# Kernel optimization log

Measured on AMD Instinct MI355X. Metric: run time of the kernel, lower is better.

The kernel has to match this reference:

```python
import jax, jax.numpy as jnp
import numpy as np
from jax.scipy.special import logsumexp

NEG = -1e9  # surrogate for -inf (keeps masking arithmetic and grads NaN-free)
ABSTRACT_PEN = 0.5


def setup_inputs() -> dict:
    key = jax.random.key(0)
    ks = jax.random.split(key, 5)
    B, T, b = 32, 256, 16
    action_logps = jax.nn.log_softmax(jax.random.normal(ks[0], (B, T, b)), axis=-1)
    stop_logps = jax.nn.log_softmax(jax.random.normal(ks[1], (B, T + 1, b, 2)), axis=-1)
    start_logps = jax.nn.log_softmax(jax.random.normal(ks[2], (B, T + 1, b)), axis=-1)
    causal_pens = jax.random.uniform(ks[3], (B, T + 1, T + 1, b))
    lengths = jax.random.randint(ks[4], (B,), 1, T + 1)
    masks = (jnp.arange(T)[None, :] < lengths[:, None]).astype(jnp.float32)
    return {"action_logps": action_logps, "stop_logps": stop_logps,
            "start_logps": start_logps, "causal_pens": causal_pens,
            "masks": masks, "lengths": lengths}


def _cc_loss(action_logps, stop_logps, start_logps, causal_pens, masks, lengths):
    B, T, b = action_logps.shape
    start_logps = start_logps - ABSTRACT_PEN
    stop_logps = stop_logps[..., ::-1]  # STOP_IX == 0 -> flip so index 1 = stop

    a_ts = jnp.swapaxes(action_logps, 0, 1)            # [T,B,b]
    stop_ts = jnp.swapaxes(stop_logps[:, 1:], 0, 1)    # [T,B,b,2]  stop_logps[:, t+1]
    start_ts = jnp.swapaxes(start_logps[:, :T], 0, 1)  # [T,B,b]
    m_ts = jnp.swapaxes(masks, 0, 1)                   # [T,B]

    # ---- cc_fw: f[t] has shape [B,b,t,2]; pad segment-start axis to T ----
    f0 = jnp.full((B, b, T, 2), NEG).at[:, 0, 0, 1].set(0.0)

    def fw_step(f_prev, xs):
        a_t, stop_t, start_t, t = xs
        # continue current option: positions < t-1
        cont = f_prev[..., 0:1] + a_t[:, :, None, None] + stop_t[:, :, None, :]
        # start a new option at position t-1
        seg = logsumexp(f_prev[..., 1], axis=(1, 2))  # [B]
        new_seg = seg[:, None, None] + start_t[:, :, None] + a_t[:, :, None] + stop_t  # [B,b,2]
        idx = jnp.arange(T)[None, None, :, None]
        f_t = jnp.where(idx == t - 1, new_seg[:, :, None, :], cont)
        return f_t, f_t

    _, F = jax.lax.scan(fw_step, f0, (a_ts, stop_ts, start_ts, jnp.arange(1, T + 1)))
    F_full = jnp.concatenate([f0[None], F], axis=0)  # [T+1,B,b,T,2]
    total_logp = logsumexp(F_full[lengths, jnp.arange(B)][..., 1], axis=(1, 2))  # [B]

    # ---- cc_bw ----
    fT = jnp.full((B, b, 2), NEG).at[:, :, 1].set(0.0)

    def bw_step(f_next, xs):
        a_t, stop_t, start_t, m_t = xs
        f0c = a_t + logsumexp(stop_t + f_next, axis=2)  # [B,b]
        f1c = logsumexp(start_t[:, :, None] + a_t[:, :, None] + stop_t + f_next, axis=(1, 2))  # [B]
        f_t = jnp.stack([f0c, jnp.broadcast_to(f1c[:, None], f0c.shape)], axis=-1)
        done = jnp.stack([jnp.full_like(f0c, NEG), jnp.zeros_like(f0c)], axis=-1)
        f_t = jnp.where(m_t[:, None, None] > 0, f_t, done)
        return f_t, f_t

    _, BW = jax.lax.scan(bw_step, fT, (a_ts, stop_ts, start_ts, m_ts), reverse=True)
    BW_full = jnp.concatenate([BW, fT[None]], axis=0)  # [T+1,B,b,2]

    # ---- causal-consistency penalty expectation ----
    # marginal[t-1, B, b, start] = fw f[t][...,1] + bw f[t][...,1]
    marg = F[..., 1] + BW_full[1:][..., 1][:, :, :, None]          # [T,B,b,T]
    probs = jnp.exp(marg - total_logp[None, :, None, None])        # padded starts -> 0
    # pen[t-1, B, b, start] = causal_pens[B, start, t, b]
    pen = jnp.transpose(causal_pens[:, :T, 1:, :], (2, 0, 3, 1))   # [T,B,b,T]
    total_cc = jnp.sum(jnp.sum(probs * pen, axis=(2, 3)) * m_ts)
    return jnp.stack([jnp.sum(total_logp), total_cc])


def reference(action_logps, stop_logps, start_logps, causal_pens, masks, lengths):
    return _cc_loss(action_logps, stop_logps, start_logps, causal_pens, masks, lengths)
```

## Files before the change

### kernel.cpp

```cpp
#include <hip/hip_runtime.h>

constexpr int B  = 32;
constexpr int T  = 256;
constexpr int NB = 16;
#define INVLN2 1.4426950408889634f
#define LN2    0.6931471805599453f
#define AP2    (0.5f * 1.4426950408889634f)

__device__ __forceinline__ float fexp2(float x) { return exp2f(x); }
__device__ __forceinline__ float flog2(float x) { return __log2f(x); }

template<int C>
__device__ __forceinline__ float dppmv(float x) {
    return __int_as_float(__builtin_amdgcn_update_dpp(
        0, __float_as_int(x), C, 0xF, 0xF, true));
}

__device__ __forceinline__ float sum16(float x) {
    x += dppmv<0xB1>(x);
    x += dppmv<0x4E>(x);
    x += dppmv<0x141>(x);
    x += dppmv<0x140>(x);
    return x;
}

__global__ __launch_bounds__(256) void scan_kernel(
    const float* __restrict__ act_g,
    const float* __restrict__ stp_g,
    const float* __restrict__ str_g,
    const int*   __restrict__ len_g,
    float* __restrict__ Wbuf,
    float* __restrict__ TLbuf,
    float* __restrict__ Ubuf,
    float* __restrict__ Vbuf,
    float* __restrict__ SSbuf,
    float* __restrict__ SBbuf)
{
    __shared__ float sm[16384];
    float* A0 = sm;
    float* A1 = sm + 4096;
    float* TB = sm + 8192;
    float* Cx = sm + 12288;
    float* Gs = TB;

    const int beta = blockIdx.x;
    const int tid  = threadIdx.x;

    const float4* a4 = (const float4*)(act_g + (size_t)beta * (T * NB));
    const float4* s4 = (const float4*)(stp_g + (size_t)beta * ((T + 1) * NB * 2) + 32);
    const float4* t4 = (const float4*)(str_g + (size_t)beta * ((T + 1) * NB));

    for (int i4 = tid; i4 < 1024; i4 += 256) {
        const int idx = i4 >> 2, q = i4 & 3;
        float4 a  = a4[i4];
        float4 sA = s4[idx * 8 + q * 2];
        float4 sB = s4[idx * 8 + q * 2 + 1];
        float4 st = t4[i4];
        float4 v0, v1, vt;
        v0.x = fexp2((a.x + sA.x) * INVLN2); v1.x = fexp2((a.x + sA.y) * INVLN2);
        v0.y = fexp2((a.y + sA.z) * INVLN2); v1.y = fexp2((a.y + sA.w) * INVLN2);
        v0.z = fexp2((a.z + sB.x) * INVLN2); v1.z = fexp2((a.z + sB.y) * INVLN2);
        v0.w = fexp2((a.w + sB.z) * INVLN2); v1.w = fexp2((a.w + sB.w) * INVLN2);
        vt.x = fexp2(st.x * INVLN2 - AP2); vt.y = fexp2(st.y * INVLN2 - AP2);
        vt.z = fexp2(st.z * INVLN2 - AP2); vt.w = fexp2(st.w * INVLN2 - AP2);
        ((float4*)A0)[i4] = v0;
        ((float4*)A1)[i4] = v1;
        ((float4*)TB)[i4] = vt;
    }
    __syncthreads();

    const int wid  = tid >> 6;
    const int lane = tid & 63;
    const int b    = lane & 15;
    const int L    = len_g[beta];

    if (wid == 0) {
        const float* A0b = A0 + b; const float* A1b = A1 + b; const float* TBb = TB + b;
        float2* ss = (float2*)(SSbuf + beta * 512);
        float E = TBb[0], Z = 0.f;
        float a0c = A0b[0],  a1c = A1b[0],  tbc = TBb[16];
        float a0n = A0b[16], a1n = A1b[16], tbn = TBb[32];
        for (int idx = 0; idx < 256; ++idx) {
            const int p = (idx + 2) & 255;
            float a0p = A0b[p * 16], a1p = A1b[p * 16], tbp = TBb[((idx + 3) & 255) * 16];
            float S = sum16(E * a0c);
            if (lane == 0) ss[idx] = make_float2(S, Z);
            if (idx < 255) {
                float En = E * a1c + S * tbc;
                unsigned e = (__float_as_uint(S) >> 23) & 0xFFu;
                E = En * __uint_as_float((254u - e) << 23);
                Z += (float)((int)e - 127);
            }
            a0c = a0n; a1c = a1n; tbc = tbn;
            a0n = a0p; a1n = a1p; tbn = tbp;
        }
    } else if (wid == 1) {
        const float* A0b = A0 + b; const float* A1b = A1 + b; const float* TBb = TB + b;
        float2* sb = (float2*)(SBbuf + beta * 512);
        float F0 = 0.f, F1 = 1.f, Z = 0.f;
        float a0c = A0b[255 * 16], a1c = A1b[255 * 16], tbc = TBb[255 * 16];
        float a0n = A0b[254 * 16], a1n = A1b[254 * 16], tbn = TBb[254 * 16];
        for (int i = 255; i >= 0; --i) {
            const int p = (i - 2) & 255;
            float a0p = A0b[p * 16], a1p = A1b[p * 16], tbp = TBb[p * 16];
            float F0n = a1c * F0 + a0c * F1;
            float F1n = sum16(tbc * F0n);
            if (lane == 0) sb[i] = make_float2(F1n, Z);
            const bool mk = (i < L);
            unsigned e = (__float_as_uint(F1n) >> 23) & 0xFFu;
            float    r = __uint_as_float((254u - e) << 23);
            F0 = mk ? F0n * r : 0.f;
            F1 = mk ? F1n * r : 1.f;
            Z  = mk ? Z + (float)((int)e - 127) : 0.f;
            a0c = a0n; a1c = a1n; tbc = tbn;
            a0n = a0p; a1n = a1p; tbn = tbp;
        }
    } else if (wid == 2) {
        const int seg = lane >> 4;
        const float* ap = act_g + (size_t)beta * 4096 + b;
        const float* sp = stp_g + (size_t)beta * 8224 + 32 + b * 2 + 1;
        float s = 0.f;
#pragma unroll 8
        for (int k = 0; k < 64; ++k) {
            const int idx = seg * 64 + k;
            s += (ap[idx * 16] + sp[idx * 32]) * INVLN2;
        }
        float inc = s;
        float u1 = __shfl_up(inc, 16); if (lane >= 16) inc += u1;
        float u2 = __shfl_up(inc, 32); if (lane >= 32) inc += u2;
        float run = inc - s;
#pragma unroll 8
        for (int k = 0; k < 64; ++k) {
            const int idx = seg * 64 + k;
            run += (ap[idx * 16] + sp[idx * 32]) * INVLN2;
            Cx[idx * 16 + b] = run;
        }
    }
    __syncthreads();

    {
        float2 sz = ((const float2*)(SSbuf + beta * 512))[tid];
        float G = flog2(sz.x) + sz.y;
        Gs[tid + 1] = G;
        if (tid == L - 1) TLbuf[beta] = G;
        if (tid >= 1) {
            float2 fz = ((const float2*)(SBbuf + beta * 512))[tid];
            Wbuf[beta * (T + 1) + tid] = (tid < L) ? flog2(fz.x) + fz.y : 0.f;
        } else {
            Wbuf[beta * (T + 1) + T] = 0.f;
        }
    }
    __syncthreads();

    float4* Ub4 = (float4*)(Ubuf + (size_t)beta * (T * NB));
    float4* Vb4 = (float4*)(Vbuf + (size_t)beta * ((T + 1) * NB));
    for (int i4 = tid; i4 < 1024; i4 += 256) {
        const int row = i4 >> 2, q = i4 & 3;
        float4 c  = ((const float4*)Cx)[i4];
        float4 sA = s4[row * 8 + q * 2];
        float4 sB = s4[row * 8 + q * 2 + 1];
        float4 V;
        V.x = c.x + (sA.x - sA.y) * INVLN2;
        V.y = c.y + (sA.z - sA.w) * INVLN2;
        V.z = c.z + (sB.x - sB.y) * INVLN2;
        V.w = c.w + (sB.z - sB.w) * INVLN2;
        Vb4[(row + 1) * 4 + q] = V;
        float4 st = t4[i4];
        float4 U;
        if (row == 0) {
            U.x = st.x * INVLN2 - AP2; U.y = st.y * INVLN2 - AP2;
            U.z = st.z * INVLN2 - AP2; U.w = st.w * INVLN2 - AP2;
        } else {
            float g = Gs[row];
            float4 cm = ((const float4*)Cx)[i4 - 4];
            U.x = g + st.x * INVLN2 - AP2 - cm.x;
            U.y = g + st.y * INVLN2 - AP2 - cm.y;
            U.z = g + st.z * INVLN2 - AP2 - cm.z;
            U.w = g + st.w * INVLN2 - AP2 - cm.w;
        }
        Ub4[i4] = U;
    }
}

__global__ __launch_bounds__(256) void cc_kernel(
    const float* __restrict__ pens,
    const int*   __restrict__ len_g,
    const float* __restrict__ Wbuf,
    const float* __restrict__ TLbuf,
    const float* __restrict__ Ubuf,
    const float* __restrict__ Vbuf,
    float* __restrict__ part)
{
    const int beta = blockIdx.x;
    const int t    = blockIdx.y + 1;
    const int tid  = threadIdx.x;
    const int pidx = blockIdx.y * B + beta;
    const int L    = len_g[beta];
    if (t > L) { if (tid == 0) part[pidx] = 0.f; return; }

    const float c0 = Wbuf[beta * (T + 1) + t] - TLbuf[beta];
    const float4* U4 = (const float4*)(Ubuf + (size_t)beta * (T * NB));
    const float4* P4 = (const float4*)(pens + (size_t)beta * ((size_t)(T+1)*(T+1)*NB)
                                            + (size_t)t * NB);
    const int q = tid & 3;
    float4 vq = ((const float4*)(Vbuf + (size_t)beta * ((T + 1) * NB) + t * NB))[q];
    vq.x += c0; vq.y += c0; vq.z += c0; vq.w += c0;

    float local = 0.f;
    const int n4 = t * 4;
    for (int i4 = tid; i4 < n4; i4 += 256) {
        const int tau = i4 >> 2;
        float4 u = U4[i4];
        float4 p = P4[(size_t)tau * ((T + 1) * 4) + (i4 & 3)];
        local += fexp2(u.x + vq.x) * p.x + fexp2(u.y + vq.y) * p.y
               + fexp2(u.z + vq.z) * p.z + fexp2(u.w + vq.w) * p.w;
    }
#pragma unroll
    for (int off = 1; off < 64; off <<= 1) local += __shfl_xor(local, off);
    __shared__ float red[4];
    if ((tid & 63) == 0) red[tid >> 6] = local;
    __syncthreads();
    if (tid == 0) part[pidx] = red[0] + red[1] + red[2] + red[3];
}

__global__ __launch_bounds__(256) void final_kernel(
    const float* __restrict__ part, const float* __restrict__ TLbuf,
    float* __restrict__ out)
{
    const int tid = threadIdx.x;
    const float4* p4 = (const float4*)part;
    float s = 0.f;
#pragma unroll
    for (int k = 0; k < 8; ++k) {
        float4 v = p4[tid + 256 * k];
        s += v.x + v.y + v.z + v.w;
    }
#pragma unroll
    for (int off = 1; off < 64; off <<= 1) s += __shfl_xor(s, off);
    __shared__ float red[4];
    if ((tid & 63) == 0) red[tid >> 6] = s;
    __syncthreads();
    if (tid == 0) out[1] = red[0] + red[1] + red[2] + red[3];

    float tl = (tid < 32) ? TLbuf[tid] : 0.f;
    if (tid < 64) {
#pragma unroll
        for (int off = 1; off < 32; off <<= 1) tl += __shfl_xor(tl, off);
        if (tid == 0) out[0] = tl * LN2;
    }
}

extern "C" void kernel_launch(void* const* d_in, const int* in_sizes, int n_in,
                              void* d_out, int out_size, void* d_ws, size_t ws_size,
                              hipStream_t stream) {
    (void)in_sizes; (void)n_in; (void)out_size; (void)ws_size;
    const float* act  = (const float*)d_in[0];
    const float* stp  = (const float*)d_in[1];
    const float* strt = (const float*)d_in[2];
    const float* pens = (const float*)d_in[3];
    const int*   lens = (const int*)d_in[5];
    float* out = (float*)d_out;

    float* ws    = (float*)d_ws;
    float* Wbuf  = ws;
    float* TLbuf = Wbuf + B * (T + 1);
    float* Ubuf  = TLbuf + B;
    float* Vbuf  = Ubuf + (size_t)B * T * NB;
    float* part  = Vbuf + (size_t)B * (T+1) * NB;
    float* SSbuf = part + T * B;
    float* SBbuf = SSbuf + B * 512;

    scan_kernel<<<B, 256, 0, stream>>>(act, stp, strt, lens, Wbuf, TLbuf, Ubuf, Vbuf, SSbuf, SBbuf);
    cc_kernel<<<dim3(B, T), 256, 0, stream>>>(pens, lens, Wbuf, TLbuf, Ubuf, Vbuf, part);
    final_kernel<<<1, 256, 0, stream>>>(part, TLbuf, out);
}
```

Before: 230.2 us.

## Merge cc blocks into 8-step chunks and drop final reduction kernel via atomics

The penalty kernel now assigns eight consecutive time steps to each block, cutting the grid from B×T to B×32 blocks and amortizing per-block setup. The separate final reduction kernel is removed: each cc block adds its partial sum atomically into the output, and the total log-probability is added atomically too, with the scan kernel zeroing the output first. This saves one launch and a global round trip, but it makes the floating-point summation order nondeterministic. It also leaves fewer blocks with unequal work, since later chunks cover longer prefixes.

```diff
diff --git a/kernel.cpp b/kernel.cpp
--- a/kernel.cpp
+++ b/kernel.cpp
@@ -34,7 +34,8 @@
     float* __restrict__ Ubuf,
     float* __restrict__ Vbuf,
     float* __restrict__ SSbuf,
-    float* __restrict__ SBbuf)
+    float* __restrict__ SBbuf,
+    float* __restrict__ out)
 {
     __shared__ float sm[16384];
     float* A0 = sm;
@@ -45,6 +46,7 @@
 
     const int beta = blockIdx.x;
     const int tid  = threadIdx.x;
+    if (beta == 0 && tid < 2) out[tid] = 0.f;
 
     const float4* a4 = (const float4*)(act_g + (size_t)beta * (T * NB));
     const float4* s4 = (const float4*)(stp_g + (size_t)beta * ((T + 1) * NB * 2) + 32);
@@ -189,65 +191,44 @@
     const float* __restrict__ TLbuf,
     const float* __restrict__ Ubuf,
     const float* __restrict__ Vbuf,
-    float* __restrict__ part)
+    float* __restrict__ out)
 {
-    const int beta = blockIdx.x;
-    const int t    = blockIdx.y + 1;
-    const int tid  = threadIdx.x;
-    const int pidx = blockIdx.y * B + beta;
-    const int L    = len_g[beta];
-    if (t > L) { if (tid == 0) part[pidx] = 0.f; return; }
-
-    const float c0 = Wbuf[beta * (T + 1) + t] - TLbuf[beta];
+    const int beta  = blockIdx.x;
+    const int chunk = blockIdx.y;
+    const int tid   = threadIdx.x;
+    const int L     = len_g[beta];
+    const int t0    = chunk * 8 + 1;
+    const float TL  = TLbuf[beta];
+    if (chunk == 0 && tid == 0) atomicAdd(out, TL * LN2);
+    if (t0 > L) return;
+
     const float4* U4 = (const float4*)(Ubuf + (size_t)beta * (T * NB));
-    const float4* P4 = (const float4*)(pens + (size_t)beta * ((size_t)(T+1)*(T+1)*NB)
-                                            + (size_t)t * NB);
+    const float*  Vb = Vbuf + (size_t)beta * ((T + 1) * NB);
+    const float*  Pb = pens + (size_t)beta * ((size_t)(T + 1) * (T + 1) * NB);
     const int q = tid & 3;
-    float4 vq = ((const float4*)(Vbuf + (size_t)beta * ((T + 1) * NB) + t * NB))[q];
-    vq.x += c0; vq.y += c0; vq.z += c0; vq.w += c0;
+    const int tend = min(t0 + 7, L);
 
     float local = 0.f;
-    const int n4 = t * 4;
-    for (int i4 = tid; i4 < n4; i4 += 256) {
-        const int tau = i4 >> 2;
-        float4 u = U4[i4];
-        float4 p = P4[(size_t)tau * ((T + 1) * 4) + (i4 & 3)];
-        local += fexp2(u.x + vq.x) * p.x + fexp2(u.y + vq.y) * p.y
-               + fexp2(u.z + vq.z) * p.z + fexp2(u.w + vq.w) * p.w;
+    for (int t = t0; t <= tend; ++t) {
+        const float c0 = Wbuf[beta * (T + 1) + t] - TL;
+        float4 vq = ((const float4*)(Vb + t * NB))[q];
+        vq.x += c0; vq.y += c0; vq.z += c0; vq.w += c0;
+        const float4* P4 = (const float4*)(Pb + (size_t)t * NB);
+        const int n4 = t * 4;
+        for (int i4 = tid; i4 < n4; i4 += 256) {
+            const int tau = i4 >> 2;
+            float4 u = U4[i4];
+            float4 p = P4[(size_t)tau * ((T + 1) * 4) + (i4 & 3)];
+            local += fexp2(u.x + vq.x) * p.x + fexp2(u.y + vq.y) * p.y
+                   + fexp2(u.z + vq.z) * p.z + fexp2(u.w + vq.w) * p.w;
+        }
     }
 #pragma unroll
     for (int off = 1; off < 64; off <<= 1) local += __shfl_xor(local, off);
     __shared__ float red[4];
     if ((tid & 63) == 0) red[tid >> 6] = local;
     __syncthreads();
-    if (tid == 0) part[pidx] = red[0] + red[1] + red[2] + red[3];
-}
-
-__global__ __launch_bounds__(256) void final_kernel(
-    const float* __restrict__ part, const float* __restrict__ TLbuf,
-    float* __restrict__ out)
-{
-    const int tid = threadIdx.x;
-    const float4* p4 = (const float4*)part;
-    float s = 0.f;
-#pragma unroll
-    for (int k = 0; k < 8; ++k) {
-        float4 v = p4[tid + 256 * k];
-        s += v.x + v.y + v.z + v.w;
-    }
-#pragma unroll
-    for (int off = 1; off < 64; off <<= 1) s += __shfl_xor(s, off);
-    __shared__ float red[4];
-    if ((tid & 63) == 0) red[tid >> 6] = s;
-    __syncthreads();
-    if (tid == 0) out[1] = red[0] + red[1] + red[2] + red[3];
-
-    float tl = (tid < 32) ? TLbuf[tid] : 0.f;
-    if (tid < 64) {
-#pragma unroll
-        for (int off = 1; off < 32; off <<= 1) tl += __shfl_xor(tl, off);
-        if (tid == 0) out[0] = tl * LN2;
-    }
+    if (tid == 0) atomicAdd(out + 1, red[0] + red[1] + red[2] + red[3]);
 }
 
 extern "C" void kernel_launch(void* const* d_in, const int* in_sizes, int n_in,
@@ -266,11 +247,9 @@
     float* TLbuf = Wbuf + B * (T + 1);
     float* Ubuf  = TLbuf + B;
     float* Vbuf  = Ubuf + (size_t)B * T * NB;
-    float* part  = Vbuf + (size_t)B * (T+1) * NB;
-    float* SSbuf = part + T * B;
+    float* SSbuf = Vbuf + (size_t)B * (T+1) * NB;
     float* SBbuf = SSbuf + B * 512;
 
-    scan_kernel<<<B, 256, 0, stream>>>(act, stp, strt, lens, Wbuf, TLbuf, Ubuf, Vbuf, SSbuf, SBbuf);
-    cc_kernel<<<dim3(B, T), 256, 0, stream>>>(pens, lens, Wbuf, TLbuf, Ubuf, Vbuf, part);
-    final_kernel<<<1, 256, 0, stream>>>(part, TLbuf, out);
-}
+    scan_kernel<<<B, 256, 0, stream>>>(act, stp, strt, lens, Wbuf, TLbuf, Ubuf, Vbuf, SSbuf, SBbuf, out);
+    cc_kernel<<<dim3(B, 32), 256, 0, stream>>>(pens, lens, Wbuf, TLbuf, Ubuf, Vbuf, out);
+}
```

New measurement: 231.6 us. About the same (+0.6%).
